# Performance work log

Measured on AMD Instinct MI355X. Metric: run time of the kernel, lower is better.

## Reference

```python
import jax, jax.numpy as jnp
import numpy as np

N, E, D_LM, H, L, C = 100000, 1000000, 1024, 128, 3, 8


def setup_inputs() -> dict:
    key = jax.random.key(0)
    ks = jax.random.split(key, 8)
    return {
        "last_hidden_state": jax.random.normal(ks[0], (N, D_LM), jnp.float32),
        "edge_index": jax.random.randint(ks[1], (2, E), 0, N, dtype=jnp.int32),
        "W_lm": jax.random.normal(ks[2], (D_LM, H), jnp.float32) * 0.03,
        "b_lm": jnp.zeros((H,), jnp.float32),
        "W_gcn": jax.random.normal(ks[3], (L, H, H), jnp.float32) * 0.08,
        "b_gcn": jnp.zeros((L, H), jnp.float32),
        "W_cls": jax.random.normal(ks[4], (2 * H, C), jnp.float32) * 0.06,
        "b_cls": jnp.zeros((C,), jnp.float32),
    }


def reference(last_hidden_state, edge_index, W_lm, b_lm, W_gcn, b_gcn, W_cls, b_cls):
    # Frozen LM output -> lm_head (dropout is identity in eval mode)
    n = last_hidden_state.shape[0]
    lm = last_hidden_state @ W_lm + b_lm                      # [N, H]

    # GCN normalization (add self-loops, symmetric deg^{-1/2} norm), shared by all layers
    loops = jnp.arange(n, dtype=edge_index.dtype)
    src = jnp.concatenate([edge_index[0], loops])             # message sources j
    dst = jnp.concatenate([edge_index[1], loops])             # aggregation targets i
    deg = jax.ops.segment_sum(jnp.ones_like(dst, jnp.float32), dst, num_segments=n)
    dinv = jax.lax.rsqrt(jnp.maximum(deg, 1.0))               # deg >= 1 due to self-loops
    norm = dinv[src] * dinv[dst]                              # [E+N]

    out = lm
    for l in range(W_gcn.shape[0]):
        h = out @ W_gcn[l]                                    # linear transform first (PyG GCNConv)
        msg = h[src] * norm[:, None]                          # gather + scale  [E+N, H]
        out = jax.ops.segment_sum(msg, dst, num_segments=n) + b_gcn[l]
        out = jax.nn.relu(out)                                # dropout identity in eval

    logits = jnp.concatenate([lm, out], axis=-1) @ W_cls + b_cls  # [N, C]
    return logits
```

## Files before the change

### kernel.cpp

```cpp
#include <hip/hip_runtime.h>


using bf16x8 = __attribute__((ext_vector_type(8))) short;
using f32x4  = __attribute__((ext_vector_type(4))) float;
typedef unsigned short u16;
typedef unsigned int   u32;

__device__ __forceinline__ u16 f2bf(float f) {
  u32 u = __builtin_bit_cast(u32, f);
  u += 0x7fffu + ((u >> 16) & 1u);
  return (u16)(u >> 16);
}
__device__ __forceinline__ float bf2f(u32 lo16) {
  return __builtin_bit_cast(float, lo16 << 16);
}
__device__ __forceinline__ u32 packbf2(float a, float b) {
  u32 r;
  asm("v_cvt_pk_bf16_f32 %0, %1, %2" : "=v"(r) : "v"(a), "v"(b));
  return r;
}
__device__ __forceinline__ void gl_lds16(const void* g, void* l) {
  __builtin_amdgcn_global_load_lds(
      (const __attribute__((address_space(1))) void*)g,
      (__attribute__((address_space(3))) void*)l, 16, 0, 0);
}


__global__ void count_kernel(const int* __restrict__ dst, int* __restrict__ counts, int E) {
  int e = blockIdx.x * 256 + threadIdx.x;
  if (e < E) atomicAdd(&counts[dst[e]], 1);
}

__global__ void dinv_kernel(const int* __restrict__ counts, float* __restrict__ dinv, int N) {
  int i = blockIdx.x * 256 + threadIdx.x;
  if (i < N) dinv[i] = rsqrtf((float)(counts[i] + 1));
}

__global__ void scan_partial(const int* __restrict__ counts, int* __restrict__ partials, int N) {
  __shared__ int sdata[256];
  int t = threadIdx.x;
  int base = blockIdx.x * 1024 + t * 4;
  int s = 0;
#pragma unroll
  for (int i = 0; i < 4; i++) { int idx = base + i; if (idx < N) s += counts[idx]; }
  sdata[t] = s; __syncthreads();
  for (int off = 128; off > 0; off >>= 1) {
    if (t < off) sdata[t] += sdata[t + off];
    __syncthreads();
  }
  if (t == 0) partials[blockIdx.x] = sdata[0];
}

__global__ void scan_partials_excl(int* __restrict__ partials, int NB,
                                   int* __restrict__ offsets, int N, int E) {
  __shared__ int sdata[256];
  int t = threadIdx.x;
  int v = (t < NB) ? partials[t] : 0;
  sdata[t] = v; __syncthreads();
  int val = v;
  for (int off = 1; off < 256; off <<= 1) {
    int add = (t >= off) ? sdata[t - off] : 0;
    __syncthreads();
    val += add; sdata[t] = val;
    __syncthreads();
  }
  if (t < NB) partials[t] = val - v;
  if (t == 0) offsets[N] = E;
}

__global__ void scan_final(const int* __restrict__ counts, const int* __restrict__ partials,
                           int* __restrict__ offsets, int N) {
  __shared__ int sdata[256];
  int t = threadIdx.x;
  int base = blockIdx.x * 1024 + t * 4;
  int v[4]; int tsum = 0;
#pragma unroll
  for (int i = 0; i < 4; i++) { int idx = base + i; v[i] = (idx < N) ? counts[idx] : 0; tsum += v[i]; }
  sdata[t] = tsum; __syncthreads();
  int val = tsum;
  for (int off = 1; off < 256; off <<= 1) {
    int add = (t >= off) ? sdata[t - off] : 0;
    __syncthreads();
    val += add; sdata[t] = val;
    __syncthreads();
  }
  int run = partials[blockIdx.x] + val - tsum;
#pragma unroll
  for (int i = 0; i < 4; i++) { int idx = base + i; if (idx < N) offsets[idx] = run; run += v[i]; }
}

__global__ void fill_kernel(const int* __restrict__ src, const int* __restrict__ dst,
                            const int* __restrict__ offsets, int* __restrict__ counts,
                            int* __restrict__ col, int E) {
  int e = blockIdx.x * 256 + threadIdx.x;
  if (e < E) {
    int d = dst[e];
    int p = offsets[d] + atomicSub(&counts[d], 1) - 1;
    col[p] = src[e];
  }
}


__global__ void prep_wlm(const float* __restrict__ W, u16* __restrict__ Wt) {
  int idx = blockIdx.x * 256 + threadIdx.x;
  if (idx < 1024 * 128) {
    int k = idx >> 7, c = idx & 127;
    Wt[c * 1024 + k] = f2bf(W[idx]);
  }
}
__global__ void prep_wgcn(const float* __restrict__ W, u16* __restrict__ Wt, int total) {
  int idx = blockIdx.x * 256 + threadIdx.x;
  if (idx < total) {
    int l = idx >> 14; int r = idx & 16383;
    int k = r >> 7, c = r & 127;
    Wt[l * 16384 + c * 128 + k] = f2bf(W[idx]);
  }
}


__global__ __launch_bounds__(256) void gemm_lm_kernel(
    const float* __restrict__ A, const u16* __restrict__ Bt,
    const float* __restrict__ bias, u16* __restrict__ Out, int Nrows)
{
  __shared__ u16 lA[2][128 * 32];
  __shared__ u16 lB[2][128 * 32];
  const int t = threadIdx.x;
  const int lane = t & 63;
  const int w = t >> 6;
  const int wr = w >> 1, wc = w & 1;
  const long rowbase = (long)blockIdx.x * 128;
  const int quad = lane >> 4;
  const int l16 = lane & 15;

  const int seg0 = t, seg1 = t + 256;
  const int r0 = seg0 >> 2, kq0 = seg0 & 3;
  const int r1 = seg1 >> 2, kq1 = seg1 & 3;
  long g0 = rowbase + r0; if (g0 >= Nrows) g0 = Nrows - 1;
  long g1 = rowbase + r1; if (g1 >= Nrows) g1 = Nrows - 1;
  const float* Ab0 = A + g0 * 1024 + kq0 * 8;
  const float* Ab1 = A + g1 * 1024 + kq1 * 8;
  const int dA0 = (seg0 * 16) ^ ((r0 & 3) << 4);
  const int dA1 = (seg1 * 16) ^ ((r1 & 3) << 4);
  const char* Bsrc0 = (const char*)Bt + (size_t)r0 * 2048 + ((kq0 ^ (r0 & 3)) << 4);
  const char* Bsrc1 = (const char*)Bt + (size_t)r1 * 2048 + ((kq1 ^ (r1 & 3)) << 4);
  const int dB0 = seg0 * 16, dB1 = seg1 * 16;

  f32x4 acc[4][4];
#pragma unroll
  for (int i = 0; i < 4; i++)
#pragma unroll
    for (int j = 0; j < 4; j++) acc[i][j] = f32x4{0.f, 0.f, 0.f, 0.f};

  float4 fa[2][4];

#define GLB(KS, BUF) do { \
    gl_lds16(Bsrc0 + (size_t)(KS) * 64, (char*)lB[BUF] + dB0); \
    gl_lds16(Bsrc1 + (size_t)(KS) * 64, (char*)lB[BUF] + dB1); \
  } while (0)

#define ALOAD(KS, S) do { \
    fa[S][0] = *reinterpret_cast<const float4*>(Ab0 + (KS) * 32); \
    fa[S][1] = *reinterpret_cast<const float4*>(Ab0 + (KS) * 32 + 4); \
    fa[S][2] = *reinterpret_cast<const float4*>(Ab1 + (KS) * 32); \
    fa[S][3] = *reinterpret_cast<const float4*>(Ab1 + (KS) * 32 + 4); \
  } while (0)

#define APACK(S, BUF) do { \
    uint4 pk0, pk1; \
    pk0.x = packbf2(fa[S][0].x, fa[S][0].y); pk0.y = packbf2(fa[S][0].z, fa[S][0].w); \
    pk0.z = packbf2(fa[S][1].x, fa[S][1].y); pk0.w = packbf2(fa[S][1].z, fa[S][1].w); \
    pk1.x = packbf2(fa[S][2].x, fa[S][2].y); pk1.y = packbf2(fa[S][2].z, fa[S][2].w); \
    pk1.z = packbf2(fa[S][3].x, fa[S][3].y); pk1.w = packbf2(fa[S][3].z, fa[S][3].w); \
    *reinterpret_cast<uint4*>((char*)lA[BUF] + dA0) = pk0; \
    *reinterpret_cast<uint4*>((char*)lA[BUF] + dA1) = pk1; \
  } while (0)

#define FRAGS(BUF) do { \
    _Pragma("unroll") \
    for (int i = 0; i < 4; i++) { \
      int r = wr * 64 + i * 16 + l16; \
      af[i] = *reinterpret_cast<const bf16x8*>( \
          (const char*)lA[BUF] + r * 64 + ((quad ^ (r & 3)) << 4)); \
    } \
    _Pragma("unroll") \
    for (int j = 0; j < 4; j++) { \
      int c = wc * 64 + j * 16 + l16; \
      bfr[j] = *reinterpret_cast<const bf16x8*>( \
          (const char*)lB[BUF] + c * 64 + ((quad ^ (c & 3)) << 4)); \
    } \
  } while (0)

#define MFMA16() do { \
    _Pragma("unroll") \
    for (int i = 0; i < 4; i++) \
      _Pragma("unroll") \
      for (int j = 0; j < 4; j++) \
        acc[i][j] = __builtin_amdgcn_mfma_f32_16x16x32_bf16(af[i], bfr[j], acc[i][j], 0, 0, 0); \
  } while (0)

  GLB(0, 0);
  ALOAD(0, 0);
  ALOAD(1, 1);
  APACK(0, 0);
  asm volatile("s_waitcnt vmcnt(0) lgkmcnt(0)" ::: "memory");
  __builtin_amdgcn_s_barrier();
  __builtin_amdgcn_sched_barrier(0);

#define STEP_FULL(KS, BUF, SPACK, SLOAD) do { \
    bf16x8 af[4], bfr[4]; \
    FRAGS(BUF); \
    GLB((KS) + 1, BUF ^ 1); \
    APACK(SPACK, BUF ^ 1); \
    ALOAD((KS) + 2, SLOAD); \
    MFMA16(); \
    asm volatile("s_waitcnt vmcnt(4) lgkmcnt(0)" ::: "memory"); \
    __builtin_amdgcn_s_barrier(); \
    __builtin_amdgcn_sched_barrier(0); \
  } while (0)

  for (int ks = 0; ks < 30; ks += 2) {
    STEP_FULL(ks, 0, 1, 0);
    STEP_FULL(ks + 1, 1, 0, 1);
  }
  {
    bf16x8 af[4], bfr[4];
    FRAGS(0);
    GLB(31, 1);
    APACK(1, 1);
    MFMA16();
    asm volatile("s_waitcnt vmcnt(0) lgkmcnt(0)" ::: "memory");
    __builtin_amdgcn_s_barrier();
    __builtin_amdgcn_sched_barrier(0);
  }
  {
    bf16x8 af[4], bfr[4];
    FRAGS(1);
    MFMA16();
  }
#undef STEP_FULL
#undef MFMA16
#undef FRAGS
#undef APACK
#undef ALOAD
#undef GLB

#pragma unroll
  for (int i = 0; i < 4; i++) {
    long rbase = rowbase + wr * 64 + i * 16 + quad * 4;
#pragma unroll
    for (int j = 0; j < 4; j++) {
      int c = wc * 64 + j * 16 + l16;
      float bv = bias[c];
#pragma unroll
      for (int r = 0; r < 4; r++) {
        long grow = rbase + r;
        if (grow < Nrows)
          Out[(size_t)grow * 128 + c] = f2bf(acc[i][j][r] + bv);
      }
    }
  }
}


__global__ __launch_bounds__(256) void gemm128_kernel(
    const u16* __restrict__ A, const u16* __restrict__ Bt,
    const float* __restrict__ rs, u16* __restrict__ Out, int Nrows)
{
  __shared__ u16 lA[128 * 128];
  __shared__ u16 lB[128 * 128];
  const int t = threadIdx.x;
  const int lane = t & 63;
  const int w = t >> 6;
  const int wr = w >> 1, wc = w & 1;
  const int row0 = blockIdx.x * 128;
  const int quad = lane >> 4;
  const int l16 = lane & 15;

#pragma unroll
  for (int rp = 0; rp < 8; rp++) {
    int o = (t + rp * 256) * 16;
    int row = o >> 8;
    int io = (o ^ ((row & 15) << 4)) & 255;
    long grow = (long)row0 + row;
    if (grow >= Nrows) grow = Nrows - 1;
    gl_lds16((const char*)A + grow * 256 + io, (char*)lA + o);
    gl_lds16((const char*)Bt + row * 256 + io, (char*)lB + o);
  }
  __syncthreads();

  f32x4 acc[4][4];
#pragma unroll
  for (int i = 0; i < 4; i++)
#pragma unroll
    for (int j = 0; j < 4; j++) acc[i][j] = f32x4{0.f, 0.f, 0.f, 0.f};

#pragma unroll
  for (int kk = 0; kk < 4; kk++) {
    bf16x8 af[4], bfr[4];
#pragma unroll
    for (int i = 0; i < 4; i++) {
      int r = wr * 64 + i * 16 + l16;
      int ch = (kk * 4 + quad) ^ (r & 15);
      af[i] = *reinterpret_cast<const bf16x8*>((const char*)lA + r * 256 + ch * 16);
    }
#pragma unroll
    for (int j = 0; j < 4; j++) {
      int c = wc * 64 + j * 16 + l16;
      int ch = (kk * 4 + quad) ^ (c & 15);
      bfr[j] = *reinterpret_cast<const bf16x8*>((const char*)lB + c * 256 + ch * 16);
    }
#pragma unroll
    for (int i = 0; i < 4; i++)
#pragma unroll
      for (int j = 0; j < 4; j++)
        acc[i][j] = __builtin_amdgcn_mfma_f32_16x16x32_bf16(af[i], bfr[j], acc[i][j], 0, 0, 0);
  }

#pragma unroll
  for (int i = 0; i < 4; i++) {
    int rbase = row0 + wr * 64 + i * 16 + quad * 4;
#pragma unroll
    for (int r = 0; r < 4; r++) {
      int grow = rbase + r;
      if (grow < Nrows) {
        float sc = rs[grow];
#pragma unroll
        for (int j = 0; j < 4; j++) {
          int c = wc * 64 + j * 16 + l16;
          Out[(size_t)grow * 128 + c] = f2bf(acc[i][j][r] * sc);
        }
      }
    }
  }
}


#define BRED(v) do { v += __shfl_xor(v, 1);  v += __shfl_xor(v, 2);  v += __shfl_xor(v, 4); \
                     v += __shfl_xor(v, 8);  v += __shfl_xor(v, 16); v += __shfl_xor(v, 32); } while (0)

template<bool FINAL>
__global__ __launch_bounds__(256) void aggregate_kernel(
    const u16* __restrict__ h, const int* __restrict__ offsets,
    const int* __restrict__ col, const float* __restrict__ dinv,
    const float* __restrict__ bias, u16* __restrict__ outf,
    const u16* __restrict__ lm, const float* __restrict__ Wc,
    const float* __restrict__ bc, float* __restrict__ logits, int N)
{
  int w = threadIdx.x >> 6;
  int lane = threadIdx.x & 63;
  int i = blockIdx.x * 4 + w;
  if (i >= N) return;
  const u32* h32 = (const u32*)h;
  u32 us = h32[(size_t)i * 64 + lane];
  float ax = bf2f(us & 0xffffu), ay = bf2f(us >> 16);
  int s = offsets[i], e = offsets[i + 1];
  for (int base = s; base < e; base += 64) {
    int cnt = e - base; if (cnt > 64) cnt = 64;
    int cj = (base + lane < e) ? col[base + lane] : 0;
    int k = 0;
    for (; k + 4 <= cnt; k += 4) {
      int j0 = __shfl(cj, k),     j1 = __shfl(cj, k + 1);
      int j2 = __shfl(cj, k + 2), j3 = __shfl(cj, k + 3);
      u32 u0 = h32[(size_t)j0 * 64 + lane];
      u32 u1 = h32[(size_t)j1 * 64 + lane];
      u32 u2 = h32[(size_t)j2 * 64 + lane];
      u32 u3 = h32[(size_t)j3 * 64 + lane];
      ax += bf2f(u0 & 0xffffu); ay += bf2f(u0 >> 16);
      ax += bf2f(u1 & 0xffffu); ay += bf2f(u1 >> 16);
      ax += bf2f(u2 & 0xffffu); ay += bf2f(u2 >> 16);
      ax += bf2f(u3 & 0xffffu); ay += bf2f(u3 >> 16);
    }
    for (; k < cnt; k++) {
      int j = __shfl(cj, k);
      u32 uu = h32[(size_t)j * 64 + lane];
      ax += bf2f(uu & 0xffffu); ay += bf2f(uu >> 16);
    }
  }
  float di = dinv[i];
  ax = fmaxf(ax * di + bias[lane * 2], 0.f);
  ay = fmaxf(ay * di + bias[lane * 2 + 1], 0.f);
  if (!FINAL) {
    ((u32*)outf)[(size_t)i * 64 + lane] = packbf2(ax, ay);
  } else {
    u32 ul = ((const u32*)lm)[(size_t)i * 64 + lane];
    float lx = bf2f(ul & 0xffffu), ly = bf2f(ul >> 16);
    const float4* W4 = (const float4*)Wc;
    float4 a0 = W4[(2 * lane) * 2],       a1 = W4[(2 * lane) * 2 + 1];
    float4 b0 = W4[(2 * lane + 1) * 2],   b1 = W4[(2 * lane + 1) * 2 + 1];
    float4 c0 = W4[(128 + 2 * lane) * 2], c1 = W4[(128 + 2 * lane) * 2 + 1];
    float4 d0 = W4[(129 + 2 * lane) * 2], d1 = W4[(129 + 2 * lane) * 2 + 1];
    float s0 = lx * a0.x + ly * b0.x + ax * c0.x + ay * d0.x;
    float s1 = lx * a0.y + ly * b0.y + ax * c0.y + ay * d0.y;
    float s2 = lx * a0.z + ly * b0.z + ax * c0.z + ay * d0.z;
    float s3 = lx * a0.w + ly * b0.w + ax * c0.w + ay * d0.w;
    float s4 = lx * a1.x + ly * b1.x + ax * c1.x + ay * d1.x;
    float s5 = lx * a1.y + ly * b1.y + ax * c1.y + ay * d1.y;
    float s6 = lx * a1.z + ly * b1.z + ax * c1.z + ay * d1.z;
    float s7 = lx * a1.w + ly * b1.w + ax * c1.w + ay * d1.w;
    BRED(s0); BRED(s1); BRED(s2); BRED(s3); BRED(s4); BRED(s5); BRED(s6); BRED(s7);
    if (lane < 8) {
      float v = s0;
      v = (lane == 1) ? s1 : v;
      v = (lane == 2) ? s2 : v;
      v = (lane == 3) ? s3 : v;
      v = (lane == 4) ? s4 : v;
      v = (lane == 5) ? s5 : v;
      v = (lane == 6) ? s6 : v;
      v = (lane == 7) ? s7 : v;
      logits[(size_t)i * 8 + lane] = v + bc[lane];
    }
  }
}
#undef BRED


static inline char* bump(char*& p, size_t bytes) {
  char* r = p;
  p += (bytes + 255) & ~(size_t)255;
  return r;
}

extern "C" void kernel_launch(void* const* d_in, const int* in_sizes, int n_in,
                              void* d_out, int out_size, void* d_ws, size_t ws_size,
                              hipStream_t stream) {
  const float* X   = (const float*)d_in[0];
  const int*   EI  = (const int*)  d_in[1];
  const float* Wlm = (const float*)d_in[2];
  const float* blm = (const float*)d_in[3];
  const float* Wg  = (const float*)d_in[4];
  const float* bg  = (const float*)d_in[5];
  const float* Wc  = (const float*)d_in[6];
  const float* bc  = (const float*)d_in[7];
  float* out = (float*)d_out;

  const int N = in_sizes[0] / 1024;
  const int E = in_sizes[1] / 2;
  const int L = in_sizes[4] / (128 * 128);

  char* wp = (char*)d_ws;
  int*   counts  = (int*)  bump(wp, (size_t)N * 4);
  int*   offs    = (int*)  bump(wp, (size_t)(N + 1) * 4);
  float* dinv    = (float*)bump(wp, (size_t)N * 4);
  int*   partials= (int*)  bump(wp, 1024 * 4);
  int*   colA    = (int*)  bump(wp, (size_t)E * 4);
  u16*   WlmT    = (u16*)  bump(wp, (size_t)1024 * 128 * 2);
  u16*   WgT     = (u16*)  bump(wp, (size_t)L * 128 * 128 * 2);
  u16*   lmB     = (u16*)  bump(wp, (size_t)N * 128 * 2);
  u16*   hB      = (u16*)  bump(wp, (size_t)N * 128 * 2);
  u16*   featB   = (u16*)  bump(wp, (size_t)N * 128 * 2);

  hipMemsetAsync(counts, 0, (size_t)N * 4, stream);

  const int* srcp = EI;
  const int* dstp = EI + E;

  count_kernel<<<(E + 255) / 256, 256, 0, stream>>>(dstp, counts, E);
  dinv_kernel<<<(N + 255) / 256, 256, 0, stream>>>(counts, dinv, N);

  int NB = (N + 1023) / 1024;
  scan_partial<<<NB, 256, 0, stream>>>(counts, partials, N);
  scan_partials_excl<<<1, 256, 0, stream>>>(partials, NB, offs, N, E);
  scan_final<<<NB, 256, 0, stream>>>(counts, partials, offs, N);
  fill_kernel<<<(E + 255) / 256, 256, 0, stream>>>(srcp, dstp, offs, counts, colA, E);

  prep_wlm<<<(1024 * 128 + 255) / 256, 256, 0, stream>>>(Wlm, WlmT);
  prep_wgcn<<<(L * 128 * 128 + 255) / 256, 256, 0, stream>>>(Wg, WgT, L * 128 * 128);

  int GB = (N + 127) / 128;
  gemm_lm_kernel<<<GB, 256, 0, stream>>>(X, WlmT, blm, lmB, N);

  const u16* cur = lmB;
  for (int l = 0; l < L; l++) {
    gemm128_kernel<<<GB, 256, 0, stream>>>(cur, WgT + (size_t)l * 16384, dinv, hB, N);
    if (l < L - 1) {
      aggregate_kernel<false><<<(N + 3) / 4, 256, 0, stream>>>(
          hB, offs, colA, dinv, bg + (size_t)l * 128, featB,
          nullptr, nullptr, nullptr, nullptr, N);
      cur = featB;
    } else {
      aggregate_kernel<true><<<(N + 3) / 4, 256, 0, stream>>>(
          hB, offs, colA, dinv, bg + (size_t)l * 128, nullptr,
          lmB, Wc, bc, out, N);
    }
  }
}
```

Before: 938.3 us.

## Fuse graph-prep kernels into GEMM launches via block-range specialization

The degree-count atomics now run as extra blocks of the LM-head GEMM launch, and the CSR fill runs as extra blocks of the first GCN GEMM. The two weight-prep kernels are merged into one launch, dinv is computed inside the partial-sum scan, and the separate partial-exclusive-scan kernel is removed because each final-scan block reduces its predecessors' partials itself. This cuts the kernel count from about fourteen to nine and lets the atomic-heavy graph work overlap with the GEMM compute. In exchange the GEMM launches carry heterogeneous blocks, and the static LDS they declare may limit how many lightweight atomic blocks can be resident at once.

```diff
diff --git a/kernel.cpp b/kernel.cpp
--- a/kernel.cpp
+++ b/kernel.cpp
@@ -26,23 +26,39 @@
 }
 
 
-__global__ void count_kernel(const int* __restrict__ dst, int* __restrict__ counts, int E) {
-  int e = blockIdx.x * 256 + threadIdx.x;
-  if (e < E) atomicAdd(&counts[dst[e]], 1);
-}
-
-__global__ void dinv_kernel(const int* __restrict__ counts, float* __restrict__ dinv, int N) {
-  int i = blockIdx.x * 256 + threadIdx.x;
-  if (i < N) dinv[i] = rsqrtf((float)(counts[i] + 1));
-}
-
-__global__ void scan_partial(const int* __restrict__ counts, int* __restrict__ partials, int N) {
+__global__ void prep_fat(const float* __restrict__ Wlm, u16* __restrict__ WlmT,
+                         const float* __restrict__ Wg, u16* __restrict__ WgT, int totalG) {
+  int b = blockIdx.x;
+  if (b < 512) {
+    int idx = b * 256 + threadIdx.x;
+    int k = idx >> 7, c = idx & 127;
+    WlmT[c * 1024 + k] = f2bf(Wlm[idx]);
+  } else {
+    int idx = (b - 512) * 256 + threadIdx.x;
+    if (idx < totalG) {
+      int l = idx >> 14; int r = idx & 16383;
+      int k = r >> 7, c = r & 127;
+      WgT[l * 16384 + c * 128 + k] = f2bf(Wg[idx]);
+    }
+  }
+}
+
+
+__global__ void dinv_scanpart(const int* __restrict__ counts, float* __restrict__ dinv,
+                              int* __restrict__ partials, int N) {
   __shared__ int sdata[256];
   int t = threadIdx.x;
   int base = blockIdx.x * 1024 + t * 4;
   int s = 0;
 #pragma unroll
-  for (int i = 0; i < 4; i++) { int idx = base + i; if (idx < N) s += counts[idx]; }
+  for (int i = 0; i < 4; i++) {
+    int idx = base + i;
+    if (idx < N) {
+      int c = counts[idx];
+      s += c;
+      dinv[idx] = rsqrtf((float)(c + 1));
+    }
+  }
   sdata[t] = s; __syncthreads();
   for (int off = 128; off > 0; off >>= 1) {
     if (t < off) sdata[t] += sdata[t + off];
@@ -51,31 +67,24 @@
   if (t == 0) partials[blockIdx.x] = sdata[0];
 }
 
-__global__ void scan_partials_excl(int* __restrict__ partials, int NB,
-                                   int* __restrict__ offsets, int N, int E) {
+
+__global__ void scan_final2(const int* __restrict__ counts, const int* __restrict__ partials,
+                            int* __restrict__ offsets, int N, int E, int NB) {
   __shared__ int sdata[256];
   int t = threadIdx.x;
-  int v = (t < NB) ? partials[t] : 0;
-  sdata[t] = v; __syncthreads();
-  int val = v;
-  for (int off = 1; off < 256; off <<= 1) {
-    int add = (t >= off) ? sdata[t - off] : 0;
+  int pv = (t < NB && t < (int)blockIdx.x) ? partials[t] : 0;
+  sdata[t] = pv; __syncthreads();
+  for (int off = 128; off > 0; off >>= 1) {
+    if (t < off) sdata[t] += sdata[t + off];
     __syncthreads();
-    val += add; sdata[t] = val;
-    __syncthreads();
-  }
-  if (t < NB) partials[t] = val - v;
-  if (t == 0) offsets[N] = E;
-}
-
-__global__ void scan_final(const int* __restrict__ counts, const int* __restrict__ partials,
-                           int* __restrict__ offsets, int N) {
-  __shared__ int sdata[256];
-  int t = threadIdx.x;
-  int base = blockIdx.x * 1024 + t * 4;
+  }
+  int bse = sdata[0];
+  __syncthreads();
+
+  int bofs = blockIdx.x * 1024 + t * 4;
   int v[4]; int tsum = 0;
 #pragma unroll
-  for (int i = 0; i < 4; i++) { int idx = base + i; v[i] = (idx < N) ? counts[idx] : 0; tsum += v[i]; }
+  for (int i = 0; i < 4; i++) { int idx = bofs + i; v[i] = (idx < N) ? counts[idx] : 0; tsum += v[i]; }
   sdata[t] = tsum; __syncthreads();
   int val = tsum;
   for (int off = 1; off < 256; off <<= 1) {
@@ -84,46 +93,25 @@
     val += add; sdata[t] = val;
     __syncthreads();
   }
-  int run = partials[blockIdx.x] + val - tsum;
-#pragma unroll
-  for (int i = 0; i < 4; i++) { int idx = base + i; if (idx < N) offsets[idx] = run; run += v[i]; }
-}
-
-__global__ void fill_kernel(const int* __restrict__ src, const int* __restrict__ dst,
-                            const int* __restrict__ offsets, int* __restrict__ counts,
-                            int* __restrict__ col, int E) {
-  int e = blockIdx.x * 256 + threadIdx.x;
-  if (e < E) {
-    int d = dst[e];
-    int p = offsets[d] + atomicSub(&counts[d], 1) - 1;
-    col[p] = src[e];
-  }
-}
-
-
-__global__ void prep_wlm(const float* __restrict__ W, u16* __restrict__ Wt) {
-  int idx = blockIdx.x * 256 + threadIdx.x;
-  if (idx < 1024 * 128) {
-    int k = idx >> 7, c = idx & 127;
-    Wt[c * 1024 + k] = f2bf(W[idx]);
-  }
-}
-__global__ void prep_wgcn(const float* __restrict__ W, u16* __restrict__ Wt, int total) {
-  int idx = blockIdx.x * 256 + threadIdx.x;
-  if (idx < total) {
-    int l = idx >> 14; int r = idx & 16383;
-    int k = r >> 7, c = r & 127;
-    Wt[l * 16384 + c * 128 + k] = f2bf(W[idx]);
-  }
-}
-
-
-__global__ __launch_bounds__(256) void gemm_lm_kernel(
+  int run = bse + val - tsum;
+#pragma unroll
+  for (int i = 0; i < 4; i++) { int idx = bofs + i; if (idx < N) offsets[idx] = run; run += v[i]; }
+  if (blockIdx.x == 0 && t == 0) offsets[N] = E;
+}
+
+
+__global__ __launch_bounds__(256) void gemm_lm_count_kernel(
     const float* __restrict__ A, const u16* __restrict__ Bt,
-    const float* __restrict__ bias, u16* __restrict__ Out, int Nrows)
+    const float* __restrict__ bias, u16* __restrict__ Out, int Nrows,
+    const int* __restrict__ dst, int* __restrict__ counts, int E, int GB)
 {
   __shared__ u16 lA[2][128 * 32];
   __shared__ u16 lB[2][128 * 32];
+  if ((int)blockIdx.x >= GB) {
+    int e = ((int)blockIdx.x - GB) * 256 + threadIdx.x;
+    if (e < E) atomicAdd(&counts[dst[e]], 1);
+    return;
+  }
   const int t = threadIdx.x;
   const int lane = t & 63;
   const int w = t >> 6;
@@ -262,17 +250,16 @@
 }
 
 
-__global__ __launch_bounds__(256) void gemm128_kernel(
+__device__ __forceinline__ void gemm128_body(
+    u16* lA, u16* lB, int bid,
     const u16* __restrict__ A, const u16* __restrict__ Bt,
     const float* __restrict__ rs, u16* __restrict__ Out, int Nrows)
 {
-  __shared__ u16 lA[128 * 128];
-  __shared__ u16 lB[128 * 128];
   const int t = threadIdx.x;
   const int lane = t & 63;
   const int w = t >> 6;
   const int wr = w >> 1, wc = w & 1;
-  const int row0 = blockIdx.x * 128;
+  const int row0 = bid * 128;
   const int quad = lane >> 4;
   const int l16 = lane & 15;
 
@@ -332,6 +319,36 @@
       }
     }
   }
+}
+
+__global__ __launch_bounds__(256) void gemm128_kernel(
+    const u16* __restrict__ A, const u16* __restrict__ Bt,
+    const float* __restrict__ rs, u16* __restrict__ Out, int Nrows)
+{
+  __shared__ u16 lA[128 * 128];
+  __shared__ u16 lB[128 * 128];
+  gemm128_body(lA, lB, blockIdx.x, A, Bt, rs, Out, Nrows);
+}
+
+__global__ __launch_bounds__(256) void gemm128_fill_kernel(
+    const u16* __restrict__ A, const u16* __restrict__ Bt,
+    const float* __restrict__ rs, u16* __restrict__ Out, int Nrows,
+    const int* __restrict__ src, const int* __restrict__ dst,
+    const int* __restrict__ offsets, int* __restrict__ counts,
+    int* __restrict__ col, int E, int GB)
+{
+  __shared__ u16 lA[128 * 128];
+  __shared__ u16 lB[128 * 128];
+  if ((int)blockIdx.x >= GB) {
+    int e = ((int)blockIdx.x - GB) * 256 + threadIdx.x;
+    if (e < E) {
+      int d = dst[e];
+      int p = offsets[d] + atomicSub(&counts[d], 1) - 1;
+      col[p] = src[e];
+    }
+    return;
+  }
+  gemm128_body(lA, lB, blockIdx.x, A, Bt, rs, Out, Nrows);
 }
 
 
@@ -454,23 +471,23 @@
   const int* srcp = EI;
   const int* dstp = EI + E;
 
-  count_kernel<<<(E + 255) / 256, 256, 0, stream>>>(dstp, counts, E);
-  dinv_kernel<<<(N + 255) / 256, 256, 0, stream>>>(counts, dinv, N);
-
-  int NB = (N + 1023) / 1024;
-  scan_partial<<<NB, 256, 0, stream>>>(counts, partials, N);
-  scan_partials_excl<<<1, 256, 0, stream>>>(partials, NB, offs, N, E);
-  scan_final<<<NB, 256, 0, stream>>>(counts, partials, offs, N);
-  fill_kernel<<<(E + 255) / 256, 256, 0, stream>>>(srcp, dstp, offs, counts, colA, E);
-
-  prep_wlm<<<(1024 * 128 + 255) / 256, 256, 0, stream>>>(Wlm, WlmT);
-  prep_wgcn<<<(L * 128 * 128 + 255) / 256, 256, 0, stream>>>(Wg, WgT, L * 128 * 128);
-
-  int GB = (N + 127) / 128;
-  gemm_lm_kernel<<<GB, 256, 0, stream>>>(X, WlmT, blm, lmB, N);
-
-  const u16* cur = lmB;
-  for (int l = 0; l < L; l++) {
+  const int GB = (N + 127) / 128;
+  const int CB = (E + 255) / 256;
+  const int NB = (N + 1023) / 1024;
+  const int PGB = (L * 128 * 128 + 255) / 256;
+
+  prep_fat<<<512 + PGB, 256, 0, stream>>>(Wlm, WlmT, Wg, WgT, L * 128 * 128);
+  gemm_lm_count_kernel<<<GB + CB, 256, 0, stream>>>(X, WlmT, blm, lmB, N, dstp, counts, E, GB);
+  dinv_scanpart<<<NB, 256, 0, stream>>>(counts, dinv, partials, N);
+  scan_final2<<<NB, 256, 0, stream>>>(counts, partials, offs, N, E, NB);
+  gemm128_fill_kernel<<<GB + CB, 256, 0, stream>>>(lmB, WgT, dinv, hB, N,
+                                                   srcp, dstp, offs, counts, colA, E, GB);
+
+  const u16* cur;
+  aggregate_kernel<false><<<(N + 3) / 4, 256, 0, stream>>>(
+      hB, offs, colA, dinv, bg, featB, nullptr, nullptr, nullptr, nullptr, N);
+  cur = featB;
+  for (int l = 1; l < L; l++) {
     gemm128_kernel<<<GB, 256, 0, stream>>>(cur, WgT + (size_t)l * 16384, dinv, hB, N);
     if (l < L - 1) {
       aggregate_kernel<false><<<(N + 3) / 4, 256, 0, stream>>>(
```

After: 886.1 us. 1.06x faster.
